# Performance work log

Measured on AMD Instinct MI355X. Metric: run time of the kernel, lower is better.

The kernel has to match this reference:

```python
import jax, jax.numpy as jnp
import numpy as np

B, L, D, N_ITEMS = 512, 100, 128, 100000
ALPHA = 0.3


def setup_inputs() -> dict:
    key = jax.random.key(0)
    ks = jax.random.split(key, 10)
    x = jax.random.randint(ks[0], (B, L), 0, N_ITEMS, dtype=jnp.int32)
    attn_mask = jnp.ones((B, L), dtype=bool)  # unused by forward (parity with torch signature)
    emb = jax.random.normal(ks[1], (N_ITEMS, D), dtype=jnp.float32) * 0.02
    emb = emb.at[0].set(0.0)  # padding_idx=0 row is zeros
    s = 1.0 / np.sqrt(D)
    W_in = jax.random.uniform(ks[2], (D, D), minval=-s, maxval=s, dtype=jnp.float32)
    W_out = jax.random.uniform(ks[3], (D, D), minval=-s, maxval=s, dtype=jnp.float32)
    w_ih = jax.random.uniform(ks[4], (3 * D, D), minval=-s, maxval=s, dtype=jnp.float32)
    w_hh = jax.random.uniform(ks[5], (3 * D, D), minval=-s, maxval=s, dtype=jnp.float32)
    b_ih = jax.random.uniform(ks[6], (3 * D,), minval=-s, maxval=s, dtype=jnp.float32)
    b_hh = jax.random.uniform(ks[7], (3 * D,), minval=-s, maxval=s, dtype=jnp.float32)
    sr = 1.0 / np.sqrt(3 * D)
    W_read = jax.random.uniform(ks[8], (D, 3 * D), minval=-sr, maxval=sr, dtype=jnp.float32)
    b_read = jax.random.uniform(ks[9], (D,), minval=-sr, maxval=sr, dtype=jnp.float32)
    return dict(x=x, attn_mask=attn_mask, emb=emb, W_in=W_in, W_out=W_out,
                w_ih=w_ih, w_hh=w_hh, b_ih=b_ih, b_hh=b_hh, W_read=W_read, b_read=b_read)


def _forward(x, emb, W_in, W_out, w_ih, w_hh, b_ih, b_hh, W_read, b_read):
    n_items, d = emb.shape
    seq_len = x.shape[1]
    BIG = n_items  # sentinel > any item id
    NEG = -1e9

    def per_sample(seq):
        valid = seq != 0
        cnt = valid.sum()
        # --- torch.unique(nonzero, return_inverse=True) via sort + dedup ---
        s = jnp.where(valid, seq, BIG)
        ss = jnp.sort(s)
        prev = jnp.concatenate([jnp.full((1,), -1, ss.dtype), ss[:-1]])
        is_first = (ss != prev) & (ss != BIG)
        n_nodes = is_first.sum()
        rank = jnp.cumsum(is_first) - 1
        nodes_s = jnp.full((seq_len,), BIG, ss.dtype).at[
            jnp.where(is_first, rank, seq_len)].set(ss, mode='drop')  # sorted unique ids, BIG-padded
        node_mask = jnp.arange(seq_len) < n_nodes
        nodes = jnp.where(node_mask, nodes_s, 0)  # pad slots -> item 0 (zero emb row)
        inv = jnp.searchsorted(nodes_s, s)  # inverse indices for valid positions
        # compact nonzero items preserving order (for consecutive-pair edges)
        pos = jnp.cumsum(valid) - 1
        cidx = jnp.where(valid, pos, seq_len)
        compact_inv = jnp.zeros((seq_len,), inv.dtype).at[cidx].set(inv, mode='drop')
        compact_seq = jnp.zeros((seq_len,), seq.dtype).at[cidx].set(seq, mode='drop')
        last_tok = compact_seq[jnp.maximum(cnt - 1, 0)]
        src, dst = compact_inv[:-1], compact_inv[1:]
        edge_mask = jnp.arange(seq_len - 1) < cnt - 1
        # --- message passing: index_add + degree normalize ---
        H0 = emb[nodes]  # [L, d]
        Hin = H0 @ W_in.T
        Hout = H0 @ W_out.T
        dst_safe = jnp.where(edge_mask, dst, seq_len)
        agg = jnp.zeros((seq_len, d), H0.dtype).at[dst_safe].add(
            jnp.where(edge_mask[:, None], Hout[src], 0.0), mode='drop')
        deg = jnp.zeros((seq_len,), H0.dtype).at[dst_safe].add(1.0, mode='drop')
        deg = jnp.maximum(deg, 1.0)
        xin = Hin + agg / deg[:, None]
        # --- GRUCell(xin, H0), torch gate order (r, z, n) ---
        gi = xin @ w_ih.T + b_ih
        gh = H0 @ w_hh.T + b_hh
        gi_r, gi_z, gi_n = jnp.split(gi, 3, axis=-1)
        gh_r, gh_z, gh_n = jnp.split(gh, 3, axis=-1)
        r = jax.nn.sigmoid(gi_r + gh_r)
        z = jax.nn.sigmoid(gi_z + gh_z)
        nct = jnp.tanh(gi_n + r * gh_n)
        H = (1.0 - z) * nct + z * H0
        H = jnp.where(node_mask[:, None], H, 0.0)  # drop padded node slots
        # --- attention readout anchored at last item ---
        li = jnp.clip(jnp.searchsorted(nodes_s, last_tok), 0, seq_len - 1)
        h_last = H[li]
        scores = jnp.where(node_mask, H @ h_last, NEG)
        att = jax.nn.softmax(scores)
        local = att @ H
        gvec = jnp.zeros((d,), H.dtype)  # cooc is None -> zeros_like(local)
        h_read = jnp.tanh(W_read @ jnp.concatenate([h_last, local, ALPHA * gvec]) + b_read)
        row = h_read @ emb.T  # tied output weights
        default = jnp.full((n_items,), NEG, row.dtype).at[0].set(0.0)
        return jnp.where(cnt >= 2, row, default)

    return jax.vmap(per_sample)(x)


def reference(x, attn_mask, emb, W_in, W_out, w_ih, w_hh, b_ih, b_hh, W_read, b_read):
    return _forward(x, emb, W_in, W_out, w_ih, w_hh, b_ih, b_hh, W_read, b_read)
```

## Files before the change

kernel.cpp:

```cpp
#include <hip/hip_runtime.h>
#include <math.h>

#define BATCH 512
#define SEQL  100
#define DIM   128
#define NITEMS 100000
#define NEGV  -1000000000.0f

#define OFF_WINT   98304
#define OFF_WOUTT  114688
#define OFF_WREADT 131072
#define OFF_HREAD  180224
#define OFF_DEG    245760
#define OFF_XIN    296960
#define OFF_HOUT   6850560
#define OFF_NODES_I 13404160
#define OFF_SRC_I   13455360
#define OFF_DST_I   13506048
#define OFF_INFO_I  13556736
#define OFF_WPACK_F 13558784

typedef __attribute__((ext_vector_type(8))) short bf16x8;
typedef __attribute__((ext_vector_type(4))) float f32x4;

__device__ __forceinline__ unsigned short bf16_rne(float x) {
  unsigned int u = __float_as_uint(x);
  unsigned int r = u + 0x7FFFu + ((u >> 16) & 1u);
  return (unsigned short)(r >> 16);
}
__device__ __forceinline__ float bf16_to_f(unsigned short h) {
  return __uint_as_float(((unsigned int)h) << 16);
}

__global__ void k_prep(const float* __restrict__ w_ih, const float* __restrict__ w_hh,
                       const float* __restrict__ W_in, const float* __restrict__ W_out,
                       const float* __restrict__ W_read, float* __restrict__ ws,
                       unsigned short* __restrict__ wpack) {
  int idx = blockIdx.x * 256 + threadIdx.x;
  if (idx < 98304) {
    int mat = idx / 49152, rem = idx % 49152;
    int n = rem / 128, k = rem % 128;
    float v = (mat ? w_hh : w_ih)[rem];
    unsigned short hi = bf16_rne(v);
    unsigned short lo = bf16_rne(v - bf16_to_f(hi));
    int nt = n >> 4, nn = n & 15, c = k >> 5, quad = (k >> 3) & 3, j = k & 7;
    int lane = quad * 16 + nn;
    size_t base = ((size_t)((mat * 24 + nt) * 4 + c)) * 1024 + (size_t)lane * 8 + j;
    wpack[base] = hi;
    wpack[base + 512] = lo;
  }
  if (idx < 49152) {
    int i = idx / 384, jj = idx % 384;
    ws[OFF_WREADT + jj * 128 + i] = W_read[idx];
  }
  if (idx < 16384) {
    int j = idx / 128, k = idx % 128;
    ws[OFF_WINT  + k * 128 + j] = W_in[idx];
    ws[OFF_WOUTT + k * 128 + j] = W_out[idx];
  }
}

__global__ void k_build(const int* __restrict__ x, int* __restrict__ nodes,
                        float* __restrict__ deg, int* __restrict__ esrc,
                        int* __restrict__ edst, int* __restrict__ info) {
  int b = blockIdx.x, tid = threadIdx.x;
  __shared__ int sseq[SEQL];
  __shared__ int sfo[SEQL];
  __shared__ unsigned char sisf[SEQL];
  __shared__ int srank[SEQL];
  __shared__ int spos[SEQL];
  __shared__ int scinv[SEQL];
  __shared__ float sdeg[SEQL];
  __shared__ int s_nn, s_cnt;

  if (tid < SEQL) sseq[tid] = x[b * SEQL + tid];
  __syncthreads();
  int t = (tid < SEQL) ? sseq[tid] : 0;
  bool valid = (tid < SEQL) && (t != 0);
  int f = tid;
  if (valid) {
    for (int j = 0; j < tid; ++j) {
      if (sseq[j] == t) { f = j; break; }
    }
  }
  if (tid < SEQL) {
    sfo[tid] = f;
    sisf[tid] = (valid && f == tid) ? 1 : 0;
    sdeg[tid] = 0.f;
  }
  __syncthreads();
  if (tid == 0) {
    int nn = 0, c = 0;
    for (int i = 0; i < SEQL; ++i) {
      srank[i] = nn; nn += sisf[i];
      spos[i] = c;  c += (sseq[i] != 0) ? 1 : 0;
    }
    s_nn = nn; s_cnt = c;
  }
  __syncthreads();
  int nn = s_nn, cnt = s_cnt;
  if (valid) scinv[spos[tid]] = srank[sfo[tid]];
  __syncthreads();
  if (tid < SEQL) {
    if (sisf[tid]) nodes[b * SEQL + srank[tid]] = t;
    if (tid >= nn) nodes[b * SEQL + tid] = 0;
  }
  __syncthreads();
  if (tid == 0) {
    int ec = (cnt >= 2) ? cnt - 1 : 0;
    for (int e = 0; e < ec; ++e) {
      int s = scinv[e], dnode = scinv[e + 1];
      esrc[b * 99 + e] = s;
      edst[b * 99 + e] = dnode;
      sdeg[dnode] += 1.f;
    }
    info[b * 4 + 0] = ec;
    info[b * 4 + 1] = (cnt >= 1) ? scinv[cnt - 1] : 0;
    info[b * 4 + 2] = (cnt >= 2) ? 1 : 0;
    info[b * 4 + 3] = nn;
  }
  __syncthreads();
  if (tid < SEQL) deg[b * SEQL + tid] = fmaxf(sdeg[tid], 1.f);
}

__global__ __launch_bounds__(256) void k_gemm_inout(
    const float* __restrict__ emb, const float* __restrict__ ws,
    const int* __restrict__ nodes, float* __restrict__ xin, float* __restrict__ hout) {
  __shared__ float Xs[64 * 128];
  int tid = threadIdx.x;
  int rowbase = blockIdx.x * 64;
  const float4* emb4 = (const float4*)emb;
  float4* Xs4 = (float4*)Xs;
  for (int e = tid; e < 64 * 32; e += 256) {
    int r = e >> 5, c4 = e & 31;
    int tok = nodes[rowbase + r];
    Xs4[e] = emb4[(size_t)tok * 32 + c4];
  }
  __syncthreads();
  int jt = tid & 31;
  int rt = tid >> 5;
  const float4* Wi4 = (const float4*)(ws + OFF_WINT);
  const float4* Wo4 = (const float4*)(ws + OFF_WOUTT);
  float accI[8][4]; float accO[8][4];
  #pragma unroll
  for (int r = 0; r < 8; ++r)
    #pragma unroll
    for (int j = 0; j < 4; ++j) { accI[r][j] = 0.f; accO[r][j] = 0.f; }

  for (int k0 = 0; k0 < 128; k0 += 4) {
    float wi[4][4], wo[4][4];
    #pragma unroll
    for (int kk = 0; kk < 4; ++kk) {
      float4 a = Wi4[(k0 + kk) * 32 + jt];
      wi[kk][0] = a.x; wi[kk][1] = a.y; wi[kk][2] = a.z; wi[kk][3] = a.w;
      float4 o = Wo4[(k0 + kk) * 32 + jt];
      wo[kk][0] = o.x; wo[kk][1] = o.y; wo[kk][2] = o.z; wo[kk][3] = o.w;
    }
    #pragma unroll
    for (int r = 0; r < 8; ++r) {
      float4 xv4 = Xs4[(rt * 8 + r) * 32 + (k0 >> 2)];
      float xv[4] = {xv4.x, xv4.y, xv4.z, xv4.w};
      #pragma unroll
      for (int kk = 0; kk < 4; ++kk)
        #pragma unroll
        for (int jj = 0; jj < 4; ++jj) {
          accI[r][jj] = fmaf(xv[kk], wi[kk][jj], accI[r][jj]);
          accO[r][jj] = fmaf(xv[kk], wo[kk][jj], accO[r][jj]);
        }
    }
  }
  float4* xin4 = (float4*)xin;
  float4* hout4 = (float4*)hout;
  #pragma unroll
  for (int r = 0; r < 8; ++r) {
    int row = rowbase + rt * 8 + r;
    float4 vI = {accI[r][0], accI[r][1], accI[r][2], accI[r][3]};
    float4 vO = {accO[r][0], accO[r][1], accO[r][2], accO[r][3]};
    xin4[(size_t)row * 32 + jt] = vI;
    hout4[(size_t)row * 32 + jt] = vO;
  }
}

__global__ void k_scatter(const float* __restrict__ hout, float* __restrict__ xin,
                          const float* __restrict__ deg, const int* __restrict__ esrc,
                          const int* __restrict__ edst, const int* __restrict__ info) {
  int b = blockIdx.x, k = threadIdx.x;
  __shared__ float agg[SEQL * DIM];
  for (int n = 0; n < SEQL; ++n) agg[n * DIM + k] = 0.f;
  int ec = info[b * 4 + 0];
  for (int e = 0; e < ec; ++e) {
    int s = esrc[b * 99 + e], dn = edst[b * 99 + e];
    agg[dn * DIM + k] += hout[((size_t)(b * SEQL + s)) * DIM + k];
  }
  for (int n = 0; n < SEQL; ++n) {
    float dg = deg[b * SEQL + n];
    size_t idx = ((size_t)(b * SEQL + n)) * DIM + k;
    xin[idx] += agg[n * DIM + k] / dg;
  }
}

#define GPAD 136
__global__ __launch_bounds__(128) void k_gru(
    const float* __restrict__ emb, const int* __restrict__ nodes,
    const unsigned short* __restrict__ wpack, const float* __restrict__ xin,
    const float* __restrict__ b_ih, const float* __restrict__ b_hh,
    const int* __restrict__ info, float* __restrict__ Hbuf) {
  __shared__ unsigned short Xhi[32 * GPAD];
  __shared__ unsigned short Xlo[32 * GPAD];
  __shared__ unsigned short Hhi[32 * GPAD];
  __shared__ unsigned short Hlo[32 * GPAD];
  int tid = threadIdx.x;
  int rowbase = blockIdx.x * 32;
  const float4* emb4 = (const float4*)emb;
  const float4* xin4 = (const float4*)xin;
  for (int e = tid; e < 32 * 32; e += 128) {
    int r = e >> 5, c4 = e & 31;
    int row = rowbase + r;
    float4 xv = xin4[(size_t)row * 32 + c4];
    int tok = nodes[row];
    float4 hv = emb4[(size_t)tok * 32 + c4];
    int base = r * GPAD + c4 * 4;
    float xs[4] = {xv.x, xv.y, xv.z, xv.w};
    float hs[4] = {hv.x, hv.y, hv.z, hv.w};
    #pragma unroll
    for (int q = 0; q < 4; ++q) {
      unsigned short xh = bf16_rne(xs[q]);
      Xhi[base + q] = xh; Xlo[base + q] = bf16_rne(xs[q] - bf16_to_f(xh));
      unsigned short hh = bf16_rne(hs[q]);
      Hhi[base + q] = hh; Hlo[base + q] = bf16_rne(hs[q] - bf16_to_f(hh));
    }
  }
  __syncthreads();
  int wave = tid >> 6, lane = tid & 63;
  int quad = lane >> 4, nIdx = lane & 15;
  int mrow = wave * 16 + nIdx;
  bf16x8 aXh[4], aXl[4], aHh[4], aHl[4];
  #pragma unroll
  for (int c = 0; c < 4; ++c) {
    int off = mrow * GPAD + c * 32 + quad * 8;
    aXh[c] = *(const bf16x8*)&Xhi[off];
    aXl[c] = *(const bf16x8*)&Xlo[off];
    aHh[c] = *(const bf16x8*)&Hhi[off];
    aHl[c] = *(const bf16x8*)&Hlo[off];
  }
  int grows[4]; int zm[4];
  #pragma unroll
  for (int i = 0; i < 4; ++i) {
    int grow = rowbase + wave * 16 + quad * 4 + i;
    grows[i] = grow;
    int bs = grow / SEQL;
    int n = grow - bs * SEQL;
    zm[i] = (n < info[bs * 4 + 3]) ? 1 : 0;
  }

  for (int t = 0; t < 8; ++t) {
    f32x4 acc[3][2];
    #pragma unroll
    for (int g = 0; g < 3; ++g)
      #pragma unroll
      for (int m = 0; m < 2; ++m) acc[g][m] = (f32x4){0.f, 0.f, 0.f, 0.f};

    for (int c = 0; c < 4; ++c) {
      bf16x8 Bh[3][2], Bl[3][2];
      #pragma unroll
      for (int g = 0; g < 3; ++g) {
        int nt = g * 8 + t;
        #pragma unroll
        for (int m = 0; m < 2; ++m) {
          size_t bidx = (size_t)((m * 24 + nt) * 4 + c) * 1024 + (size_t)lane * 8;
          Bh[g][m] = *(const bf16x8*)&wpack[bidx];
          Bl[g][m] = *(const bf16x8*)&wpack[bidx + 512];
        }
      }
      #pragma unroll
      for (int g = 0; g < 3; ++g) {
        acc[g][0] = __builtin_amdgcn_mfma_f32_16x16x32_bf16(aXh[c], Bh[g][0], acc[g][0], 0, 0, 0);
        acc[g][1] = __builtin_amdgcn_mfma_f32_16x16x32_bf16(aHh[c], Bh[g][1], acc[g][1], 0, 0, 0);
      }
      #pragma unroll
      for (int g = 0; g < 3; ++g) {
        acc[g][0] = __builtin_amdgcn_mfma_f32_16x16x32_bf16(aXh[c], Bl[g][0], acc[g][0], 0, 0, 0);
        acc[g][1] = __builtin_amdgcn_mfma_f32_16x16x32_bf16(aHh[c], Bl[g][1], acc[g][1], 0, 0, 0);
      }
      #pragma unroll
      for (int g = 0; g < 3; ++g) {
        acc[g][0] = __builtin_amdgcn_mfma_f32_16x16x32_bf16(aXl[c], Bh[g][0], acc[g][0], 0, 0, 0);
        acc[g][1] = __builtin_amdgcn_mfma_f32_16x16x32_bf16(aHl[c], Bh[g][1], acc[g][1], 0, 0, 0);
      }
    }
    int j = t * 16 + nIdx;
    float biR = b_ih[j],       bhR = b_hh[j];
    float biZ = b_ih[128 + j], bhZ = b_hh[128 + j];
    float biN = b_ih[256 + j], bhN = b_hh[256 + j];
    #pragma unroll
    for (int i = 0; i < 4; ++i) {
      float gr = acc[0][0][i] + biR + acc[0][1][i] + bhR;
      float gz = acc[1][0][i] + biZ + acc[1][1][i] + bhZ;
      float r = 1.f / (1.f + expf(-gr));
      float z = 1.f / (1.f + expf(-gz));
      float nct = tanhf(acc[2][0][i] + biN + r * (acc[2][1][i] + bhN));
      int lrow = wave * 16 + quad * 4 + i;
      float h0 = bf16_to_f(Hhi[lrow * GPAD + j]) + bf16_to_f(Hlo[lrow * GPAD + j]);
      float h = (1.f - z) * nct + z * h0;
      if (!zm[i]) h = 0.f;
      Hbuf[(size_t)grows[i] * 128 + j] = h;
    }
  }
}

#define HLS 129
__global__ void k_attn(const float* __restrict__ Hbuf, const float* __restrict__ ws,
                       const float* __restrict__ b_read, const int* __restrict__ info,
                       float* __restrict__ hread) {
  int b = blockIdx.x, tid = threadIdx.x;
  __shared__ float Hl[SEQL * HLS];
  __shared__ float sc[128];
  __shared__ float hl[128];
  __shared__ float att[SEQL];
  __shared__ float loc[128];
  int nn = info[b * 4 + 3], li = info[b * 4 + 1];
  for (int e = tid; e < SEQL * 128; e += 128) {
    int r = e >> 7, k = e & 127;
    Hl[r * HLS + k] = Hbuf[((size_t)(b * SEQL + r)) * DIM + k];
  }
  __syncthreads();
  hl[tid] = Hl[li * HLS + tid];
  __syncthreads();
  float scr = NEGV;
  if (tid < nn) {
    float s = 0.f;
    for (int k = 0; k < 128; ++k) s += Hl[tid * HLS + k] * hl[k];
    scr = s;
  }
  sc[tid] = scr;
  __syncthreads();
  if (tid == 0) {
    float m = sc[0];
    for (int n = 1; n < SEQL; ++n) m = fmaxf(m, sc[n]);
    float sum = 0.f;
    for (int n = 0; n < SEQL; ++n) { float e = expf(sc[n] - m); att[n] = e; sum += e; }
    float inv = 1.f / sum;
    for (int n = 0; n < SEQL; ++n) att[n] *= inv;
  }
  __syncthreads();
  float lv = 0.f;
  for (int n = 0; n < SEQL; ++n) lv = fmaf(att[n], Hl[n * HLS + tid], lv);
  loc[tid] = lv;
  __syncthreads();
  const float* WrT = ws + OFF_WREADT;
  float acc = b_read[tid];
  for (int j = 0; j < 128; ++j) acc = fmaf(WrT[j * 128 + tid], hl[j], acc);
  for (int j = 0; j < 128; ++j) acc = fmaf(WrT[(128 + j) * 128 + tid], loc[j], acc);
  hread[b * 128 + tid] = tanhf(acc);
}

__global__ __launch_bounds__(256) void k_out(
    const float* __restrict__ emb, const float* __restrict__ hread,
    const int* __restrict__ info, float* __restrict__ out) {
  __shared__ float Es[8][132];
  __shared__ float Hs[8][132];
  int tid = threadIdx.x;
  int b0  = blockIdx.x * 128;
  int it0 = blockIdx.y * 128;
  int ti = (tid & 15) * 8;
  int tb = (tid >> 4) * 8;

  const float4* emb4 = (const float4*)emb;
  const float4* hr4  = (const float4*)hread;
  int li = tid >> 1;
  int lh = tid & 1;

  float acc[8][8];
  #pragma unroll
  for (int bt = 0; bt < 8; ++bt)
    #pragma unroll
    for (int q = 0; q < 8; ++q) acc[bt][q] = 0.f;

  int item = it0 + li;
  float4 e4 = {0.f, 0.f, 0.f, 0.f};
  if (item < NITEMS) e4 = emb4[(size_t)item * 32 + lh];
  float4 h4 = hr4[(size_t)(b0 + li) * 32 + lh];

  for (int k0 = 0; k0 < 128; k0 += 8) {
    __syncthreads();
    Es[4 * lh + 0][li] = e4.x; Es[4 * lh + 1][li] = e4.y;
    Es[4 * lh + 2][li] = e4.z; Es[4 * lh + 3][li] = e4.w;
    Hs[4 * lh + 0][li] = h4.x; Hs[4 * lh + 1][li] = h4.y;
    Hs[4 * lh + 2][li] = h4.z; Hs[4 * lh + 3][li] = h4.w;
    __syncthreads();
    if (k0 + 8 < 128) {
      int kq = ((k0 + 8) >> 2) + lh;
      e4 = (item < NITEMS) ? emb4[(size_t)item * 32 + kq]
                           : (float4){0.f, 0.f, 0.f, 0.f};
      h4 = hr4[(size_t)(b0 + li) * 32 + kq];
    }
    #pragma unroll
    for (int kk = 0; kk < 8; ++kk) {
      float4 ev0 = *(const float4*)&Es[kk][ti];
      float4 ev1 = *(const float4*)&Es[kk][ti + 4];
      float4 hv0 = *(const float4*)&Hs[kk][tb];
      float4 hv1 = *(const float4*)&Hs[kk][tb + 4];
      float ev[8] = {ev0.x, ev0.y, ev0.z, ev0.w, ev1.x, ev1.y, ev1.z, ev1.w};
      float hv[8] = {hv0.x, hv0.y, hv0.z, hv0.w, hv1.x, hv1.y, hv1.z, hv1.w};
      #pragma unroll
      for (int bt = 0; bt < 8; ++bt)
        #pragma unroll
        for (int q = 0; q < 8; ++q)
          acc[bt][q] = fmaf(hv[bt], ev[q], acc[bt][q]);
    }
  }

  #pragma unroll
  for (int bt = 0; bt < 8; ++bt) {
    int b = b0 + tb + bt;
    int flag = info[b * 4 + 2];
    int itb = it0 + ti;
    #pragma unroll
    for (int qs = 0; qs < 2; ++qs) {
      int it = itb + qs * 4;
      if (it >= NITEMS) continue;
      float4 v;
      if (flag) {
        v.x = acc[bt][qs * 4 + 0]; v.y = acc[bt][qs * 4 + 1];
        v.z = acc[bt][qs * 4 + 2]; v.w = acc[bt][qs * 4 + 3];
      } else {
        v.x = (it == 0) ? 0.f : NEGV; v.y = NEGV; v.z = NEGV; v.w = NEGV;
      }
      *(float4*)&out[(size_t)b * NITEMS + it] = v;
    }
  }
}

extern "C" void kernel_launch(void* const* d_in, const int* in_sizes, int n_in,
                              void* d_out, int out_size, void* d_ws, size_t ws_size,
                              hipStream_t stream) {
  const int*   x      = (const int*)d_in[0];
  const float* emb    = (const float*)d_in[2];
  const float* W_in   = (const float*)d_in[3];
  const float* W_out  = (const float*)d_in[4];
  const float* w_ih   = (const float*)d_in[5];
  const float* w_hh   = (const float*)d_in[6];
  const float* b_ih   = (const float*)d_in[7];
  const float* b_hh   = (const float*)d_in[8];
  const float* W_read = (const float*)d_in[9];
  const float* b_read = (const float*)d_in[10];
  float* ws  = (float*)d_ws;
  int*   wsi = (int*)d_ws;
  unsigned short* wpack = (unsigned short*)(ws + OFF_WPACK_F);
  float* out = (float*)d_out;

  k_prep<<<384, 256, 0, stream>>>(w_ih, w_hh, W_in, W_out, W_read, ws, wpack);
  k_build<<<BATCH, 128, 0, stream>>>(x, wsi + OFF_NODES_I, ws + OFF_DEG,
                                     wsi + OFF_SRC_I, wsi + OFF_DST_I, wsi + OFF_INFO_I);
  k_gemm_inout<<<800, 256, 0, stream>>>(emb, ws, wsi + OFF_NODES_I,
                                        ws + OFF_XIN, ws + OFF_HOUT);
  k_scatter<<<BATCH, 128, 0, stream>>>(ws + OFF_HOUT, ws + OFF_XIN, ws + OFF_DEG,
                                       wsi + OFF_SRC_I, wsi + OFF_DST_I, wsi + OFF_INFO_I);
  k_gru<<<1600, 128, 0, stream>>>(emb, wsi + OFF_NODES_I, wpack, ws + OFF_XIN,
                                  b_ih, b_hh, wsi + OFF_INFO_I, ws + OFF_HOUT);
  k_attn<<<BATCH, 128, 0, stream>>>(ws + OFF_HOUT, ws, b_read, wsi + OFF_INFO_I,
                                    ws + OFF_HREAD);
  k_out<<<dim3(4, 782), 256, 0, stream>>>(emb, ws + OFF_HREAD, wsi + OFF_INFO_I, out);
}
```

Baseline: 574.2 us.

## Move output logits GEMM to bf16 MFMA with hi/lo split precision

Replaces the FP32 FMA-tiled output projection (hread @ emb^T) with MFMA bf16 16x16x32 instructions. Both operands are split into bf16 hi and lo parts and three products are accumulated to keep near-fp32 accuracy. A new k_packA kernel pre-packs hread into MFMA fragment layout in reused workspace. The emb tile is converted to hi/lo in LDS per block, and the item tile shrinks to 64. The output stores become scalar per element rather than float4, which may hurt write coalescing on this large, write-bound output.

```diff
diff --git a/kernel.cpp b/kernel.cpp
--- a/kernel.cpp
+++ b/kernel.cpp
@@ -21,6 +21,7 @@
 #define OFF_WPACK_F 13558784
 
 typedef __attribute__((ext_vector_type(8))) short bf16x8;
+typedef __attribute__((ext_vector_type(4))) short s16x4;
 typedef __attribute__((ext_vector_type(4))) float f32x4;
 
 __device__ __forceinline__ unsigned short bf16_rne(float x) {
@@ -354,81 +355,120 @@
   hread[b * 128 + tid] = tanhf(acc);
 }
 
+__global__ __launch_bounds__(256) void k_packA(
+    const float* __restrict__ hread, unsigned short* __restrict__ apack) {
+  int idx = blockIdx.x * 256 + threadIdx.x;
+  if (idx >= 8192) return;
+  int lane = idx & 63;
+  int kc = (idx >> 6) & 3;
+  int mt = idx >> 8;
+  int quad = lane >> 4, rr = lane & 15;
+  int row = mt * 16 + rr;
+  int kbase = kc * 32 + quad * 8;
+  const float4* hr4 = (const float4*)(hread + row * 128 + kbase);
+  float4 v0 = hr4[0], v1 = hr4[1];
+  float vs[8] = {v0.x, v0.y, v0.z, v0.w, v1.x, v1.y, v1.z, v1.w};
+  bf16x8 hi, lo;
+  #pragma unroll
+  for (int j = 0; j < 8; ++j) {
+    unsigned short h = bf16_rne(vs[j]);
+    hi[j] = (short)h;
+    lo[j] = (short)bf16_rne(vs[j] - bf16_to_f(h));
+  }
+  size_t base = ((size_t)(mt * 4 + kc) * 2) * 512 + (size_t)lane * 8;
+  *(bf16x8*)&apack[base] = hi;
+  *(bf16x8*)&apack[base + 512] = lo;
+}
+
+#define EPITCH 136
 __global__ __launch_bounds__(256) void k_out(
-    const float* __restrict__ emb, const float* __restrict__ hread,
+    const float* __restrict__ emb, const unsigned short* __restrict__ apack,
     const int* __restrict__ info, float* __restrict__ out) {
-  __shared__ float Es[8][132];
-  __shared__ float Hs[8][132];
+  __shared__ unsigned short Ehi[64 * EPITCH];
+  __shared__ unsigned short Elo[64 * EPITCH];
   int tid = threadIdx.x;
   int b0  = blockIdx.x * 128;
-  int it0 = blockIdx.y * 128;
-  int ti = (tid & 15) * 8;
-  int tb = (tid >> 4) * 8;
+  int it0 = blockIdx.y * 64;
 
   const float4* emb4 = (const float4*)emb;
-  const float4* hr4  = (const float4*)hread;
-  int li = tid >> 1;
-  int lh = tid & 1;
-
-  float acc[8][8];
-  #pragma unroll
-  for (int bt = 0; bt < 8; ++bt)
-    #pragma unroll
-    for (int q = 0; q < 8; ++q) acc[bt][q] = 0.f;
-
-  int item = it0 + li;
-  float4 e4 = {0.f, 0.f, 0.f, 0.f};
-  if (item < NITEMS) e4 = emb4[(size_t)item * 32 + lh];
-  float4 h4 = hr4[(size_t)(b0 + li) * 32 + lh];
-
-  for (int k0 = 0; k0 < 128; k0 += 8) {
-    __syncthreads();
-    Es[4 * lh + 0][li] = e4.x; Es[4 * lh + 1][li] = e4.y;
-    Es[4 * lh + 2][li] = e4.z; Es[4 * lh + 3][li] = e4.w;
-    Hs[4 * lh + 0][li] = h4.x; Hs[4 * lh + 1][li] = h4.y;
-    Hs[4 * lh + 2][li] = h4.z; Hs[4 * lh + 3][li] = h4.w;
-    __syncthreads();
-    if (k0 + 8 < 128) {
-      int kq = ((k0 + 8) >> 2) + lh;
-      e4 = (item < NITEMS) ? emb4[(size_t)item * 32 + kq]
-                           : (float4){0.f, 0.f, 0.f, 0.f};
-      h4 = hr4[(size_t)(b0 + li) * 32 + kq];
-    }
-    #pragma unroll
-    for (int kk = 0; kk < 8; ++kk) {
-      float4 ev0 = *(const float4*)&Es[kk][ti];
-      float4 ev1 = *(const float4*)&Es[kk][ti + 4];
-      float4 hv0 = *(const float4*)&Hs[kk][tb];
-      float4 hv1 = *(const float4*)&Hs[kk][tb + 4];
-      float ev[8] = {ev0.x, ev0.y, ev0.z, ev0.w, ev1.x, ev1.y, ev1.z, ev1.w};
-      float hv[8] = {hv0.x, hv0.y, hv0.z, hv0.w, hv1.x, hv1.y, hv1.z, hv1.w};
-      #pragma unroll
-      for (int bt = 0; bt < 8; ++bt)
-        #pragma unroll
-        for (int q = 0; q < 8; ++q)
-          acc[bt][q] = fmaf(hv[bt], ev[q], acc[bt][q]);
-    }
-  }
-
-  #pragma unroll
-  for (int bt = 0; bt < 8; ++bt) {
-    int b = b0 + tb + bt;
-    int flag = info[b * 4 + 2];
-    int itb = it0 + ti;
-    #pragma unroll
-    for (int qs = 0; qs < 2; ++qs) {
-      int it = itb + qs * 4;
-      if (it >= NITEMS) continue;
-      float4 v;
-      if (flag) {
-        v.x = acc[bt][qs * 4 + 0]; v.y = acc[bt][qs * 4 + 1];
-        v.z = acc[bt][qs * 4 + 2]; v.w = acc[bt][qs * 4 + 3];
-      } else {
-        v.x = (it == 0) ? 0.f : NEGV; v.y = NEGV; v.z = NEGV; v.w = NEGV;
+  #pragma unroll
+  for (int s = 0; s < 8; ++s) {
+    int idx = s * 256 + tid;
+    int r = idx >> 5, c4 = idx & 31;
+    int item = it0 + r;
+    float4 v = (item < NITEMS) ? emb4[(size_t)item * 32 + c4]
+                               : (float4){0.f, 0.f, 0.f, 0.f};
+    float vs[4] = {v.x, v.y, v.z, v.w};
+    s16x4 hv, lv;
+    #pragma unroll
+    for (int q = 0; q < 4; ++q) {
+      unsigned short h = bf16_rne(vs[q]);
+      hv[q] = (short)h;
+      lv[q] = (short)bf16_rne(vs[q] - bf16_to_f(h));
+    }
+    int base = r * EPITCH + c4 * 4;
+    *(s16x4*)&Ehi[base] = hv;
+    *(s16x4*)&Elo[base] = lv;
+  }
+  __syncthreads();
+
+  int wave = tid >> 6, lane = tid & 63;
+  int quad = lane >> 4, nIdx = lane & 15;
+  int mtg0 = blockIdx.x * 8 + wave * 2;
+
+  bf16x8 ah[2][4], al[2][4];
+  #pragma unroll
+  for (int m2 = 0; m2 < 2; ++m2)
+    #pragma unroll
+    for (int kc = 0; kc < 4; ++kc) {
+      size_t base = ((size_t)((mtg0 + m2) * 4 + kc) * 2) * 512 + (size_t)lane * 8;
+      ah[m2][kc] = *(const bf16x8*)&apack[base];
+      al[m2][kc] = *(const bf16x8*)&apack[base + 512];
+    }
+
+  f32x4 acc[2][4];
+  #pragma unroll
+  for (int m2 = 0; m2 < 2; ++m2)
+    #pragma unroll
+    for (int nt = 0; nt < 4; ++nt) acc[m2][nt] = (f32x4){0.f, 0.f, 0.f, 0.f};
+
+  #pragma unroll
+  for (int nt = 0; nt < 4; ++nt) {
+    int eoff = (nt * 16 + nIdx) * EPITCH + quad * 8;
+    #pragma unroll
+    for (int kc = 0; kc < 4; ++kc) {
+      bf16x8 Bh = *(const bf16x8*)&Ehi[eoff + kc * 32];
+      bf16x8 Bl = *(const bf16x8*)&Elo[eoff + kc * 32];
+      acc[0][nt] = __builtin_amdgcn_mfma_f32_16x16x32_bf16(ah[0][kc], Bh, acc[0][nt], 0, 0, 0);
+      acc[1][nt] = __builtin_amdgcn_mfma_f32_16x16x32_bf16(ah[1][kc], Bh, acc[1][nt], 0, 0, 0);
+      acc[0][nt] = __builtin_amdgcn_mfma_f32_16x16x32_bf16(al[0][kc], Bh, acc[0][nt], 0, 0, 0);
+      acc[1][nt] = __builtin_amdgcn_mfma_f32_16x16x32_bf16(al[1][kc], Bh, acc[1][nt], 0, 0, 0);
+      acc[0][nt] = __builtin_amdgcn_mfma_f32_16x16x32_bf16(ah[0][kc], Bl, acc[0][nt], 0, 0, 0);
+      acc[1][nt] = __builtin_amdgcn_mfma_f32_16x16x32_bf16(ah[1][kc], Bl, acc[1][nt], 0, 0, 0);
+    }
+  }
+
+  int flags[2][4];
+  #pragma unroll
+  for (int m2 = 0; m2 < 2; ++m2)
+    #pragma unroll
+    for (int i = 0; i < 4; ++i) {
+      int b = b0 + (wave * 2 + m2) * 16 + quad * 4 + i;
+      flags[m2][i] = info[b * 4 + 2];
+    }
+  #pragma unroll
+  for (int m2 = 0; m2 < 2; ++m2)
+    #pragma unroll
+    for (int nt = 0; nt < 4; ++nt) {
+      int item = it0 + nt * 16 + nIdx;
+      #pragma unroll
+      for (int i = 0; i < 4; ++i) {
+        int b = b0 + (wave * 2 + m2) * 16 + quad * 4 + i;
+        float v = flags[m2][i] ? acc[m2][nt][i]
+                               : ((item == 0) ? 0.f : NEGV);
+        if (item < NITEMS) out[(size_t)b * NITEMS + item] = v;
       }
-      *(float4*)&out[(size_t)b * NITEMS + it] = v;
-    }
-  }
+    }
 }
 
 extern "C" void kernel_launch(void* const* d_in, const int* in_sizes, int n_in,
@@ -447,6 +487,7 @@
   float* ws  = (float*)d_ws;
   int*   wsi = (int*)d_ws;
   unsigned short* wpack = (unsigned short*)(ws + OFF_WPACK_F);
+  unsigned short* apack = (unsigned short*)(ws + OFF_XIN);
   float* out = (float*)d_out;
 
   k_prep<<<384, 256, 0, stream>>>(w_ih, w_hh, W_in, W_out, W_read, ws, wpack);
@@ -460,5 +501,6 @@
                                   b_ih, b_hh, wsi + OFF_INFO_I, ws + OFF_HOUT);
   k_attn<<<BATCH, 128, 0, stream>>>(ws + OFF_HOUT, ws, b_read, wsi + OFF_INFO_I,
                                     ws + OFF_HREAD);
-  k_out<<<dim3(4, 782), 256, 0, stream>>>(emb, ws + OFF_HREAD, wsi + OFF_INFO_I, out);
-}
+  k_packA<<<32, 256, 0, stream>>>(ws + OFF_HREAD, apack);
+  k_out<<<dim3(4, 1563), 256, 0, stream>>>(emb, apack, wsi + OFF_INFO_I, out);
+}
```

New measurement: 506.5 us. 11.8% less time.
